# Performance work log

Measured on AMD Instinct MI355X. Metric: run time of the kernel, lower is better.

## Reference

```python
import jax, jax.numpy as jnp
import numpy as np

MIN_NORM = 1e-15
BALL_EPS = 4e-3   # HGCN float32 projection epsilon
MAX_NORM = 1e6    # manifold.max_norm used in torch.clamp(max=...)
C = 1.0           # c_in == c_out
N, E, D = 50000, 800000, 128


def artanh(x):
    return jnp.arctanh(jnp.clip(x, -1.0 + 1e-7, 1.0 - 1e-7))


def _norm(x):
    return jnp.clip(jnp.linalg.norm(x, axis=-1, keepdims=True), MIN_NORM)


def proj(x, c):
    # clip points to stay inside the Poincare ball of curvature c
    sc = c ** 0.5
    n = _norm(x)
    maxn = (1.0 - BALL_EPS) / sc
    return jnp.where(n > maxn, x / n * maxn, x)


def expmap0(u, c):
    sc = c ** 0.5
    n = _norm(u)
    return jnp.tanh(sc * n) * u / (sc * n)


def logmap0(p, c):
    sc = c ** 0.5
    n = _norm(p)
    return artanh(sc * n) * p / (sc * n)


def mobius_matvec(w, x, c):
    sc = c ** 0.5
    xn = _norm(x)
    mx = x @ w.T                      # [N, D_out]
    mxn = _norm(mx)
    res = jnp.tanh(mxn / xn * artanh(sc * xn)) * mx / (mxn * sc)
    zero = jnp.all(mx == 0, axis=-1, keepdims=True)
    return jnp.where(zero, jnp.zeros_like(res), res)


def mobius_add(x, y, c):
    x2 = jnp.sum(x * x, -1, keepdims=True)
    y2 = jnp.sum(y * y, -1, keepdims=True)
    xy = jnp.sum(x * y, -1, keepdims=True)
    num = (1 + 2 * c * xy + c * y2) * x + (1 - c * x2) * y
    den = 1 + 2 * c * xy + c * c * x2 * y2
    return num / jnp.clip(den, MIN_NORM)


def setup_inputs() -> dict:
    key = jax.random.key(0)
    k1, k2, k3, k4, k5 = jax.random.split(key, 5)
    # valid Poincare-ball points: expmap0 of small tangent vectors
    xt = 0.1 * jax.random.normal(k1, (N, D), jnp.float32)
    x = proj(expmap0(xt, C), C)
    edge_row = jax.random.randint(k2, (E,), 0, N)
    edge_col = jax.random.randint(k3, (E,), 0, N)
    adj_val = jax.random.uniform(k4, (E,), jnp.float32) / 16.0  # ~normalized adjacency weights
    weight = jax.random.normal(k5, (D, D), jnp.float32) * (2.0 / D) ** 0.5  # xavier, gain sqrt(2)
    bias = jnp.full((D,), 1e-4, jnp.float32)  # init.constant_(bias, 0.0001)
    return {"x": x, "adj_val": adj_val, "weight": weight, "bias": bias,
            "edge_row": edge_row, "edge_col": edge_col}


def reference(x, adj_val, weight, bias, edge_row, edge_col):
    c = C
    # ---- HypLinear (eval mode: no dropout) ----
    h = proj(mobius_matvec(weight, x, c), c)
    hyp_bias = proj(expmap0(bias[None, :], c), c)  # proj_tan0 is identity on the ball
    h = proj(mobius_add(h, hyp_bias, c), c)
    # ---- HypAgg (spmm path) ----
    x_tangent = logmap0(h, c)                                     # [N, D]
    msgs = adj_val[:, None] * x_tangent[edge_col]                 # [E, D] gather
    support_t = jax.ops.segment_sum(msgs, edge_row, num_segments=N)
    support_t = jnp.minimum(support_t, MAX_NORM)                  # clamp(max=max_norm)
    h = proj(expmap0(support_t, c), c)
    # ---- HypAct (relu in tangent space at origin) ----
    xt = jnp.minimum(jax.nn.relu(logmap0(h, c)), MAX_NORM)
    out = expmap0(xt, c)  # c_out == c_in; HypAct does not re-project
    return out
```

## Files before the change

kernel.cpp:

```cpp
#include <hip/hip_runtime.h>

#define D 128
#define MAXN 0.996f
#define MINN 1e-15f
#define ARTANH_MAX (1.0f - 1e-7f)
#define MAX_NORM 1e6f

typedef unsigned int uint;
typedef unsigned short ushort;
typedef __bf16 bf16x8 __attribute__((ext_vector_type(8)));
typedef float f32x4 __attribute__((ext_vector_type(4)));

__device__ __forceinline__ float quad_sum(float v) {
    v += __shfl_xor(v, 16, 64);
    v += __shfl_xor(v, 32, 64);
    return v;
}

__device__ __forceinline__ float half_sum32(float v) {
    v += __shfl_xor(v, 16, 64);
    v += __shfl_xor(v, 8, 64);
    v += __shfl_xor(v, 4, 64);
    v += __shfl_xor(v, 2, 64);
    v += __shfl_xor(v, 1, 64);
    return v;
}

__device__ __forceinline__ float artanh_clip(float x) {
    x = fminf(fmaxf(x, -ARTANH_MAX), ARTANH_MAX);
    return 0.5f * logf((1.0f + x) / (1.0f - x));
}

__device__ __forceinline__ ushort f2bf(float f) {
    uint u = __float_as_uint(f);
    return (ushort)((u + 0x7fffu + ((u >> 16) & 1u)) >> 16);
}

__device__ __forceinline__ uint pk2(float a, float b) {
    return (uint)f2bf(a) | ((uint)f2bf(b) << 16);
}

__global__ __launch_bounds__(256)
void wconv_kernel(const float* __restrict__ W, uint4* __restrict__ WF,
                  int4* __restrict__ cnt4, int n4)
{
    int idx = blockIdx.x * 256 + threadIdx.x;
    if (idx < 2048) {
        int l = idx & 63, rest = idx >> 6;
        int t = rest & 7, ks = rest >> 3;
        int lr = l & 15, kg = l >> 4;
        const float* wrow = W + (size_t)(t * 16 + lr) * D + ks * 32 + kg * 4;
        float4 lo = *(const float4*)(wrow);
        float4 hi = *(const float4*)(wrow + 16);
        WF[idx] = make_uint4(pk2(lo.x, lo.y), pk2(lo.z, lo.w),
                             pk2(hi.x, hi.y), pk2(hi.z, hi.w));
    }
    for (int z = idx; z < n4; z += gridDim.x * 256)
        cnt4[z] = make_int4(0, 0, 0, 0);
}

__global__ __launch_bounds__(128)
void gemm_mfma_kernel(const float* __restrict__ X, const uint4* __restrict__ WF,
                      const float* __restrict__ bias, ushort* __restrict__ XT, int N)
{
    const int wid = threadIdx.x >> 6;
    const int l   = threadIdx.x & 63;
    const int m0  = (blockIdx.x * 2 + wid) * 16;
    if (m0 >= N) return;
    const int lr = l & 15;
    const int kg = l >> 4;
    const int row = m0 + lr;
    const int rowc = row < N ? row : N - 1;

    const float* xp = X + (size_t)rowc * D + kg * 4;
    bf16x8 bfr[4];
    float xsq = 0.f;
#pragma unroll
    for (int ks = 0; ks < 4; ++ks) {
        float4 v0 = *(const float4*)(xp + ks * 32);
        float4 v1 = *(const float4*)(xp + ks * 32 + 16);
        xsq += v0.x*v0.x + v0.y*v0.y + v0.z*v0.z + v0.w*v0.w
             + v1.x*v1.x + v1.y*v1.y + v1.z*v1.z + v1.w*v1.w;
        uint4 bq = make_uint4(pk2(v0.x, v0.y), pk2(v0.z, v0.w),
                              pk2(v1.x, v1.y), pk2(v1.z, v1.w));
        bfr[ks] = __builtin_bit_cast(bf16x8, bq);
    }
    xsq = quad_sum(xsq);

    f32x4 acc[8];
#pragma unroll
    for (int t = 0; t < 8; ++t) acc[t] = (f32x4){0.f, 0.f, 0.f, 0.f};
#pragma unroll
    for (int ks = 0; ks < 4; ++ks) {
        uint4 wv[8];
#pragma unroll
        for (int t = 0; t < 8; ++t) wv[t] = WF[(ks * 8 + t) * 64 + l];
#pragma unroll
        for (int t = 0; t < 8; ++t)
            acc[t] = __builtin_amdgcn_mfma_f32_16x16x32_bf16(
                __builtin_bit_cast(bf16x8, wv[t]), bfr[ks], acc[t], 0, 0, 0);
    }

    float4 bb[8];
    float bsq = 0.f;
#pragma unroll
    for (int t = 0; t < 8; ++t) {
        bb[t] = *(const float4*)(bias + t * 16 + kg * 4);
        bsq += bb[t].x*bb[t].x + bb[t].y*bb[t].y + bb[t].z*bb[t].z + bb[t].w*bb[t].w;
    }
    bsq = quad_sum(bsq);
    float bn  = fmaxf(sqrtf(bsq), MINN);
    float bt  = tanhf(bn);
    float bps = (bt > MAXN) ? MAXN / fmaxf(bt, MINN) : 1.0f;
    float bsc = bt / bn * bps;
    float bhn = fminf(fmaxf(bt * bps, MINN), MAXN);
    float y2  = bhn * bhn;

    float sacc = 0.f, sab = 0.f;
#pragma unroll
    for (int t = 0; t < 8; ++t) {
        sacc += acc[t][0]*acc[t][0] + acc[t][1]*acc[t][1] + acc[t][2]*acc[t][2] + acc[t][3]*acc[t][3];
        sab  += acc[t][0]*bb[t].x + acc[t][1]*bb[t].y + acc[t][2]*bb[t].z + acc[t][3]*bb[t].w;
    }
    sacc = quad_sum(sacc);
    sab  = quad_sum(sab);

    float xn  = fmaxf(sqrtf(xsq), MINN);
    float mxn = fmaxf(sqrtf(sacc), MINN);
    float t1  = tanhf(mxn / xn * artanh_clip(xn));
    float s1  = t1 / mxn;
    float ps1 = (t1 > MAXN) ? MAXN / fmaxf(t1, MINN) : 1.0f;
    float s1p = s1 * ps1;
    float rn  = fminf(fmaxf(t1, MINN), MAXN);
    float x2  = rn * rn;
    float mxb = bsc * sab;
    float xy  = s1p * mxb;
    float ca  = 1.0f + 2.0f * xy + y2;
    float cb  = 1.0f - x2;
    float den = fmaxf(1.0f + 2.0f * xy + x2 * y2, MINN);
    float alpha = ca * s1p / den;
    float beta  = cb / den;
    float hn2 = alpha * alpha * sacc + 2.0f * alpha * beta * mxb + beta * beta * y2;
    float hn  = fmaxf(sqrtf(hn2), MINN);
    float ps2 = (hn > MAXN) ? MAXN / hn : 1.0f;
    float hnc = fmaxf(fminf(hn, MAXN), MINN);
    float ls  = artanh_clip(hnc) / hnc;
    float F   = ls * ps2;
    float A = F * alpha, Bc = F * beta * bsc;

    if (row < N) {
        ushort* op = XT + (size_t)row * D + kg * 4;
#pragma unroll
        for (int t = 0; t < 8; ++t) {
            uint2 o = make_uint2(pk2(A * acc[t][0] + Bc * bb[t].x, A * acc[t][1] + Bc * bb[t].y),
                                 pk2(A * acc[t][2] + Bc * bb[t].z, A * acc[t][3] + Bc * bb[t].w));
            *(uint2*)(op + t * 16) = o;
        }
    }
}

__global__ __launch_bounds__(256)
void hist_kernel(const int* __restrict__ erow, int* __restrict__ cnt,
                 int* __restrict__ rank, int E)
{
    int e4 = blockIdx.x * 256 + threadIdx.x;
    int E4 = E >> 2;
    if (e4 < E4) {
        int4 r = ((const int4*)erow)[e4];
        int4 k;
        k.x = atomicAdd(&cnt[r.x], 1);
        k.y = atomicAdd(&cnt[r.y], 1);
        k.z = atomicAdd(&cnt[r.z], 1);
        k.w = atomicAdd(&cnt[r.w], 1);
        ((int4*)rank)[e4] = k;
    }
    if (e4 == 0) {
        for (int i = E4 * 4; i < E; ++i) rank[i] = atomicAdd(&cnt[erow[i]], 1);
    }
}

__global__ __launch_bounds__(256)
void scan1_kernel(const int* __restrict__ cnt, int* __restrict__ offs,
                  int* __restrict__ bsum, int N)
{
    __shared__ int wsum[4];
    int t = threadIdx.x;
    int base = blockIdx.x * 1024 + t * 4;
    int v[4];
#pragma unroll
    for (int j = 0; j < 4; ++j) v[j] = (base + j < N) ? cnt[base + j] : 0;
    int tt = v[0] + v[1] + v[2] + v[3];
    int incl = tt;
#pragma unroll
    for (int o = 1; o < 64; o <<= 1) {
        int n = __shfl_up(incl, o, 64);
        if ((t & 63) >= o) incl += n;
    }
    if ((t & 63) == 63) wsum[t >> 6] = incl;
    __syncthreads();
    int wbase = 0;
    for (int w = 0; w < (t >> 6); ++w) wbase += wsum[w];
    int ex = wbase + incl - tt;
#pragma unroll
    for (int j = 0; j < 4; ++j) {
        if (base + j < N) offs[base + j] = ex;
        ex += v[j];
    }
    if (t == 255) bsum[blockIdx.x] = wbase + incl;
}

__global__ __launch_bounds__(64)
void scan2_kernel(int* __restrict__ bsum, int nb)
{
    int l = threadIdx.x;
    int v = (l < nb) ? bsum[l] : 0;
    int incl = v;
#pragma unroll
    for (int o = 1; o < 64; o <<= 1) {
        int n = __shfl_up(incl, o, 64);
        if (l >= o) incl += n;
    }
    if (l < nb) bsum[l] = incl - v;
}

__global__ __launch_bounds__(256)
void fill_kernel(const int* __restrict__ erow, const int* __restrict__ ecol,
                 const float* __restrict__ adj, const int* __restrict__ rank,
                 const int* __restrict__ offs, const int* __restrict__ bsum,
                 uint* __restrict__ bpack, int E)
{
    int e4 = blockIdx.x * 256 + threadIdx.x;
    int E4 = E >> 2;
    if (e4 < E4) {
        int4   r = ((const int4*)erow)[e4];
        int4   c = ((const int4*)ecol)[e4];
        float4 a = ((const float4*)adj)[e4];
        int4   k = ((const int4*)rank)[e4];
        bpack[offs[r.x] + bsum[r.x >> 10] + k.x] = ((uint)c.x << 16) | (uint)f2bf(a.x);
        bpack[offs[r.y] + bsum[r.y >> 10] + k.y] = ((uint)c.y << 16) | (uint)f2bf(a.y);
        bpack[offs[r.z] + bsum[r.z >> 10] + k.z] = ((uint)c.z << 16) | (uint)f2bf(a.z);
        bpack[offs[r.w] + bsum[r.w >> 10] + k.w] = ((uint)c.w << 16) | (uint)f2bf(a.w);
    }
    if (e4 == 0) {
        for (int i = E4 * 4; i < E; ++i) {
            int r = erow[i];
            bpack[offs[r] + bsum[r >> 10] + rank[i]] = ((uint)ecol[i] << 16) | (uint)f2bf(adj[i]);
        }
    }
}

__global__ __launch_bounds__(256)
void gather_kernel(const ushort* __restrict__ XT, const uint* __restrict__ bpack,
                   const int* __restrict__ offs, const int* __restrict__ bsum,
                   const int* __restrict__ cnt, float* __restrict__ OUT, int N)
{
    int row = blockIdx.x * 4 + (threadIdx.x >> 6);
    int lane = threadIdx.x & 63;
    if (row >= N) return;
    int start = offs[row] + bsum[row >> 10];
    int end = start + cnt[row];
    const uint2* xt2 = (const uint2*)XT;
    const int hl = lane & 31;
    const int hi = lane >> 5;
    float a0[4] = {0.f, 0.f, 0.f, 0.f};
    float a1[4] = {0.f, 0.f, 0.f, 0.f};
    float a2[4] = {0.f, 0.f, 0.f, 0.f};
    float a3[4] = {0.f, 0.f, 0.f, 0.f};
    int i = start;
    for (; i + 7 < end; i += 8) {
        uint4 qa = *(const uint4*)(bpack + i);
        uint4 qb = *(const uint4*)(bpack + i + 4);
        uint q0 = hi ? qa.y : qa.x;
        uint q1 = hi ? qa.w : qa.z;
        uint q2 = hi ? qb.y : qb.x;
        uint q3 = hi ? qb.w : qb.z;
        uint2 u0 = xt2[(size_t)(q0 >> 16) * 32 + hl];
        uint2 u1 = xt2[(size_t)(q1 >> 16) * 32 + hl];
        uint2 u2 = xt2[(size_t)(q2 >> 16) * 32 + hl];
        uint2 u3 = xt2[(size_t)(q3 >> 16) * 32 + hl];
        float v0 = __uint_as_float(q0 << 16);
        float v1 = __uint_as_float(q1 << 16);
        float v2 = __uint_as_float(q2 << 16);
        float v3 = __uint_as_float(q3 << 16);
        a0[0] += v0 * __uint_as_float(u0.x << 16);
        a0[1] += v0 * __uint_as_float(u0.x & 0xffff0000u);
        a0[2] += v0 * __uint_as_float(u0.y << 16);
        a0[3] += v0 * __uint_as_float(u0.y & 0xffff0000u);
        a1[0] += v1 * __uint_as_float(u1.x << 16);
        a1[1] += v1 * __uint_as_float(u1.x & 0xffff0000u);
        a1[2] += v1 * __uint_as_float(u1.y << 16);
        a1[3] += v1 * __uint_as_float(u1.y & 0xffff0000u);
        a2[0] += v2 * __uint_as_float(u2.x << 16);
        a2[1] += v2 * __uint_as_float(u2.x & 0xffff0000u);
        a2[2] += v2 * __uint_as_float(u2.y << 16);
        a2[3] += v2 * __uint_as_float(u2.y & 0xffff0000u);
        a3[0] += v3 * __uint_as_float(u3.x << 16);
        a3[1] += v3 * __uint_as_float(u3.x & 0xffff0000u);
        a3[2] += v3 * __uint_as_float(u3.y << 16);
        a3[3] += v3 * __uint_as_float(u3.y & 0xffff0000u);
    }
    for (; i + 1 < end; i += 2) {
        uint2 qp = *(const uint2*)(bpack + i);
        uint q = hi ? qp.y : qp.x;
        uint2 u = xt2[(size_t)(q >> 16) * 32 + hl];
        float v = __uint_as_float(q << 16);
        a0[0] += v * __uint_as_float(u.x << 16);
        a0[1] += v * __uint_as_float(u.x & 0xffff0000u);
        a0[2] += v * __uint_as_float(u.y << 16);
        a0[3] += v * __uint_as_float(u.y & 0xffff0000u);
    }
    if (i < end) {
        uint q = bpack[i];
        uint2 u = xt2[(size_t)(q >> 16) * 32 + hl];
        float v = hi ? 0.f : __uint_as_float(q << 16);
        a1[0] += v * __uint_as_float(u.x << 16);
        a1[1] += v * __uint_as_float(u.x & 0xffff0000u);
        a1[2] += v * __uint_as_float(u.y << 16);
        a1[3] += v * __uint_as_float(u.y & 0xffff0000u);
    }
    float c0 = (a0[0] + a1[0]) + (a2[0] + a3[0]);
    float c1 = (a0[1] + a1[1]) + (a2[1] + a3[1]);
    float c2 = (a0[2] + a1[2]) + (a2[2] + a3[2]);
    float c3 = (a0[3] + a1[3]) + (a2[3] + a3[3]);
    c0 += __shfl_xor(c0, 32, 64);
    c1 += __shfl_xor(c1, 32, 64);
    c2 += __shfl_xor(c2, 32, 64);
    c3 += __shfl_xor(c3, 32, 64);
    c0 = fminf(c0, MAX_NORM); c1 = fminf(c1, MAX_NORM);
    c2 = fminf(c2, MAX_NORM); c3 = fminf(c3, MAX_NORM);
    float nt = fmaxf(sqrtf(half_sum32(c0*c0 + c1*c1 + c2*c2 + c3*c3)), MINN);
    float th = tanhf(nt);
    float es = th / nt;
    float pf = (th > MAXN) ? MAXN / th : 1.0f;
    float hnc = fmaxf(fminf(th, MAXN), MINN);
    float ls = artanh_clip(hnc) / hnc;
    float su = ls * pf * es;
    float u0 = fminf(fmaxf(su * c0, 0.0f), MAX_NORM);
    float u1 = fminf(fmaxf(su * c1, 0.0f), MAX_NORM);
    float u2 = fminf(fmaxf(su * c2, 0.0f), MAX_NORM);
    float u3 = fminf(fmaxf(su * c3, 0.0f), MAX_NORM);
    float un = fmaxf(sqrtf(half_sum32(u0*u0 + u1*u1 + u2*u2 + u3*u3)), MINN);
    float os = tanhf(un) / un;
    if (hi == 0)
        *(float4*)(OUT + (size_t)row * D + hl * 4) =
            make_float4(os * u0, os * u1, os * u2, os * u3);
}

extern "C" void kernel_launch(void* const* d_in, const int* in_sizes, int n_in,
                              void* d_out, int out_size, void* d_ws, size_t ws_size,
                              hipStream_t stream)
{
    const float* x    = (const float*)d_in[0];
    const float* adj  = (const float*)d_in[1];
    const float* W    = (const float*)d_in[2];
    const float* bias = (const float*)d_in[3];
    const int*   erow = (const int*)d_in[4];
    const int*   ecol = (const int*)d_in[5];
    float* out = (float*)d_out;
    const int N = in_sizes[0] / D;
    const int E = in_sizes[1];

    char* p = (char*)d_ws;
    size_t off = 0;
    auto alloc = [&](size_t bytes) {
        char* r = p + off;
        off = (off + bytes + 255) & ~(size_t)255;
        return r;
    };
    ushort* xt  = (ushort*)alloc((size_t)N * D * sizeof(ushort));
    uint4*  wf  = (uint4*) alloc(2048 * sizeof(uint4));
    int*   cnt  = (int*)  alloc(((size_t)N + 4) * sizeof(int));
    int*   offs = (int*)  alloc((size_t)N * sizeof(int));
    int*   bsum = (int*)  alloc(256 * sizeof(int));
    int*   rank = (int*)  alloc((size_t)E * sizeof(int));
    uint*  bpack= (uint*) alloc((size_t)E * sizeof(uint));
    (void)ws_size;

    int n4 = (N + 3) >> 2;
    wconv_kernel<<<64, 256, 0, stream>>>(W, wf, (int4*)cnt, n4);
    gemm_mfma_kernel<<<(N + 31) / 32, 128, 0, stream>>>(x, wf, bias, xt, N);
    int E4 = E >> 2;
    hist_kernel<<<(E4 + 255) / 256, 256, 0, stream>>>(erow, cnt, rank, E);
    int nb = (N + 1023) / 1024;
    scan1_kernel<<<nb, 256, 0, stream>>>(cnt, offs, bsum, N);
    scan2_kernel<<<1, 64, 0, stream>>>(bsum, nb);
    fill_kernel<<<(E4 + 255) / 256, 256, 0, stream>>>(erow, ecol, adj, rank, offs, bsum, bpack, E);
    gather_kernel<<<(N + 3) / 4, 256, 0, stream>>>(xt, bpack, offs, bsum, cnt, out, N);
}
```

Measured before the change: 118.3 us.

## Fuse GEMM with edge histogram and fold block-sum scan into last scan block

Merges the MFMA GEMM kernel and the row histogram kernel into one launch, with block indices partitioned between the two roles. Each GEMM block now covers four waves instead of two, so the GEMM and the atomic-heavy histogram can run concurrently. The second-level scan kernel is removed: the last block to finish scan1, found through an atomic counter and thread fences, scans the block sums itself. This removes two kernel launches and their dependency gaps, at the cost of a counter that must be reset each call and some added fence overhead.

```diff
diff --git a/kernel.cpp b/kernel.cpp
--- a/kernel.cpp
+++ b/kernel.cpp
@@ -42,7 +42,7 @@
 
 __global__ __launch_bounds__(256)
 void wconv_kernel(const float* __restrict__ W, uint4* __restrict__ WF,
-                  int4* __restrict__ cnt4, int n4)
+                  int4* __restrict__ cnt4, int n4, int* __restrict__ done)
 {
     int idx = blockIdx.x * 256 + threadIdx.x;
     if (idx < 2048) {
@@ -55,17 +55,37 @@
         WF[idx] = make_uint4(pk2(lo.x, lo.y), pk2(lo.z, lo.w),
                              pk2(hi.x, hi.y), pk2(hi.z, hi.w));
     }
+    if (idx == 0) *done = 0;
     for (int z = idx; z < n4; z += gridDim.x * 256)
         cnt4[z] = make_int4(0, 0, 0, 0);
 }
 
-__global__ __launch_bounds__(128)
-void gemm_mfma_kernel(const float* __restrict__ X, const uint4* __restrict__ WF,
-                      const float* __restrict__ bias, ushort* __restrict__ XT, int N)
-{
+__global__ __launch_bounds__(256)
+void phase1_kernel(const float* __restrict__ X, const uint4* __restrict__ WF,
+                   const float* __restrict__ bias, ushort* __restrict__ XT, int N, int G,
+                   const int* __restrict__ erow, int* __restrict__ cnt,
+                   int* __restrict__ rank, int E)
+{
+    if ((int)blockIdx.x >= G) {
+        int e4 = (blockIdx.x - G) * 256 + threadIdx.x;
+        int E4 = E >> 2;
+        if (e4 < E4) {
+            int4 r = ((const int4*)erow)[e4];
+            int4 k;
+            k.x = atomicAdd(&cnt[r.x], 1);
+            k.y = atomicAdd(&cnt[r.y], 1);
+            k.z = atomicAdd(&cnt[r.z], 1);
+            k.w = atomicAdd(&cnt[r.w], 1);
+            ((int4*)rank)[e4] = k;
+        }
+        if (e4 == 0) {
+            for (int i = E4 * 4; i < E; ++i) rank[i] = atomicAdd(&cnt[erow[i]], 1);
+        }
+        return;
+    }
     const int wid = threadIdx.x >> 6;
     const int l   = threadIdx.x & 63;
-    const int m0  = (blockIdx.x * 2 + wid) * 16;
+    const int m0  = (blockIdx.x * 4 + wid) * 16;
     if (m0 >= N) return;
     const int lr = l & 15;
     const int kg = l >> 4;
@@ -160,30 +180,11 @@
 }
 
 __global__ __launch_bounds__(256)
-void hist_kernel(const int* __restrict__ erow, int* __restrict__ cnt,
-                 int* __restrict__ rank, int E)
-{
-    int e4 = blockIdx.x * 256 + threadIdx.x;
-    int E4 = E >> 2;
-    if (e4 < E4) {
-        int4 r = ((const int4*)erow)[e4];
-        int4 k;
-        k.x = atomicAdd(&cnt[r.x], 1);
-        k.y = atomicAdd(&cnt[r.y], 1);
-        k.z = atomicAdd(&cnt[r.z], 1);
-        k.w = atomicAdd(&cnt[r.w], 1);
-        ((int4*)rank)[e4] = k;
-    }
-    if (e4 == 0) {
-        for (int i = E4 * 4; i < E; ++i) rank[i] = atomicAdd(&cnt[erow[i]], 1);
-    }
-}
-
-__global__ __launch_bounds__(256)
 void scan1_kernel(const int* __restrict__ cnt, int* __restrict__ offs,
-                  int* __restrict__ bsum, int N)
+                  int* __restrict__ bsum, int* __restrict__ done, int N, int nb)
 {
     __shared__ int wsum[4];
+    __shared__ int islast;
     int t = threadIdx.x;
     int base = blockIdx.x * 1024 + t * 4;
     int v[4];
@@ -207,20 +208,22 @@
         ex += v[j];
     }
     if (t == 255) bsum[blockIdx.x] = wbase + incl;
-}
-
-__global__ __launch_bounds__(64)
-void scan2_kernel(int* __restrict__ bsum, int nb)
-{
-    int l = threadIdx.x;
-    int v = (l < nb) ? bsum[l] : 0;
-    int incl = v;
-#pragma unroll
-    for (int o = 1; o < 64; o <<= 1) {
-        int n = __shfl_up(incl, o, 64);
-        if (l >= o) incl += n;
-    }
-    if (l < nb) bsum[l] = incl - v;
+    __threadfence();
+    if (t == 255) islast = (atomicAdd(done, 1) == nb - 1);
+    __syncthreads();
+    if (islast) {
+        __threadfence();
+        if (t < 64) {
+            int bv = (t < nb) ? bsum[t] : 0;
+            int incl2 = bv;
+#pragma unroll
+            for (int o = 1; o < 64; o <<= 1) {
+                int n = __shfl_up(incl2, o, 64);
+                if (t >= o) incl2 += n;
+            }
+            if (t < nb) bsum[t] = incl2 - bv;
+        }
+    }
 }
 
 __global__ __launch_bounds__(256)
@@ -372,18 +375,21 @@
     int*   cnt  = (int*)  alloc(((size_t)N + 4) * sizeof(int));
     int*   offs = (int*)  alloc((size_t)N * sizeof(int));
     int*   bsum = (int*)  alloc(256 * sizeof(int));
+    int*   done = (int*)  alloc(256);
     int*   rank = (int*)  alloc((size_t)E * sizeof(int));
     uint*  bpack= (uint*) alloc((size_t)E * sizeof(uint));
     (void)ws_size;
 
     int n4 = (N + 3) >> 2;
-    wconv_kernel<<<64, 256, 0, stream>>>(W, wf, (int4*)cnt, n4);
-    gemm_mfma_kernel<<<(N + 31) / 32, 128, 0, stream>>>(x, wf, bias, xt, N);
+    wconv_kernel<<<64, 256, 0, stream>>>(W, wf, (int4*)cnt, n4, done);
+
     int E4 = E >> 2;
-    hist_kernel<<<(E4 + 255) / 256, 256, 0, stream>>>(erow, cnt, rank, E);
+    int G = (N + 63) / 64;
+    int H = (E4 + 255) / 256;
+    phase1_kernel<<<G + H, 256, 0, stream>>>(x, wf, bias, xt, N, G, erow, cnt, rank, E);
+
     int nb = (N + 1023) / 1024;
-    scan1_kernel<<<nb, 256, 0, stream>>>(cnt, offs, bsum, N);
-    scan2_kernel<<<1, 64, 0, stream>>>(bsum, nb);
+    scan1_kernel<<<nb, 256, 0, stream>>>(cnt, offs, bsum, done, N, nb);
     fill_kernel<<<(E4 + 255) / 256, 256, 0, stream>>>(erow, ecol, adj, rank, offs, bsum, bpack, E);
     gather_kernel<<<(N + 3) / 4, 256, 0, stream>>>(xt, bpack, offs, bsum, cnt, out, N);
 }
```

Measured after the change: 124.2 us. +5.0%, slower.
